# Optimization experiments

Hardware: AMD Instinct MI355X
Metric: run time of the kernel (lower is better)

## Reference

```python
import jax, jax.numpy as jnp
import numpy as np
from jax import lax

B, S, V, E, H, L = 256, 512, 32, 128, 512, 4  # batch, seq, vocab, embed, rnn_units, layers


def _lstm_bias(n4h):
    # Keras unit_forget_bias=True: forget-gate slice initialized to 1.
    b = jnp.zeros((n4h,), jnp.float32)
    return b.at[n4h // 4: n4h // 2].set(1.0)


def setup_inputs() -> dict:
    key = jax.random.key(0)
    ks = jax.random.split(key, 10)
    g = lambda k, shape, sc=0.02: (jax.random.normal(k, shape, jnp.float32) * sc)
    return dict(
        tokens=jax.random.randint(ks[0], (B, S), 0, V),
        emb=g(ks[1], (V, E), 0.05),
        w0=g(ks[2], (E, 4 * H)),
        u0=g(ks[3], (H, 4 * H)),
        b0=_lstm_bias(4 * H),
        w_rest=g(ks[4], (L - 1, H, 4 * H)),
        u_rest=g(ks[5], (L - 1, H, 4 * H)),
        b_rest=jnp.tile(_lstm_bias(4 * H)[None], (L - 1, 1)),
        dw1=g(ks[6], (H, 2 * H)),
        db1=jnp.zeros((2 * H,), jnp.float32),
        dw2=g(ks[7], (2 * H, V)),
        db2=jnp.zeros((V,), jnp.float32),
    )


def _lstm_layer(x, W, U, b):
    # x: [B,S,D]. Precompute input projection once (big GEMM), scan the recurrence.
    xz = jnp.einsum('bsd,dk->bsk', x, W) + b  # [B,S,4H]
    h0 = jnp.zeros((x.shape[0], H), x.dtype)
    c0 = jnp.zeros_like(h0)

    def step(carry, z_t):
        h, c = carry
        z = z_t + h @ U                      # [B,4H]
        i, f, g, o = jnp.split(z, 4, axis=-1)  # Keras gate order i,f,c,o
        i = jax.nn.sigmoid(i)
        f = jax.nn.sigmoid(f)
        g = jnp.tanh(g)
        o = jax.nn.sigmoid(o)
        c = f * c + i * g
        h = o * jnp.tanh(c)
        return (h, c), h

    _, hs = lax.scan(step, (h0, c0), jnp.swapaxes(xz, 0, 1))  # time-major scan
    return jnp.swapaxes(hs, 0, 1)  # [B,S,H]


def reference(tokens, emb, w0, u0, b0, w_rest, u_rest, b_rest, dw1, db1, dw2, db2):
    x = emb[tokens] * jnp.sqrt(jnp.float32(E))  # embedding scaled by sqrt(embedding_dim)
    x = _lstm_layer(x, w0, u0, b0)
    for i in range(L - 1):  # fixed small layer loop
        x = _lstm_layer(x, w_rest[i], u_rest[i], b_rest[i])
    h = jax.nn.relu(jnp.einsum('bsh,hk->bsk', x, dw1) + db1)
    return jnp.einsum('bsk,kv->bsv', h, dw2) + db2  # logits [B,S,V]
```

## Files before the change

### kernel.cpp

```cpp
#include <hip/hip_runtime.h>
#include <stdint.h>

#define NB 256
#define NS 512
#define NV 32
#define NE 128
#define NH 512
#define N4H 2048

typedef __attribute__((ext_vector_type(8))) short short8;
typedef __attribute__((ext_vector_type(4))) float f32x4;
typedef __attribute__((ext_vector_type(4))) unsigned int u32x4;
typedef __attribute__((ext_vector_type(4))) unsigned short u16x4;

__device__ __forceinline__ float bf2f(unsigned short u){
  unsigned int x = ((unsigned int)u) << 16;
  return __builtin_bit_cast(float, x);
}
__device__ __forceinline__ unsigned short f2bf(float f){
  unsigned int u = __builtin_bit_cast(unsigned int, f);
  u += 0x7fffu + ((u >> 16) & 1u);
  return (unsigned short)(u >> 16);
}
__device__ __forceinline__ void gload_lds16(const void* g, void* l){
  __builtin_amdgcn_global_load_lds(
      (const __attribute__((address_space(1))) unsigned int*)(uintptr_t)g,
      (__attribute__((address_space(3))) unsigned int*)(uintptr_t)l,
      16, 0, 0);
}

__global__ __launch_bounds__(256) void transpose_cast(
    const float* __restrict__ in, unsigned short* __restrict__ out, int K, int N)
{
  int k = blockIdx.x * 256 + threadIdx.x;
  int n = blockIdx.y;
  if (k < K) out[(long)n * K + k] = f2bf(in[(long)k * N + n]);
}

__global__ __launch_bounds__(256) void embed_kernel(
    const int* __restrict__ tok, const float* __restrict__ emb,
    unsigned short* __restrict__ x0)
{
  long gid = (long)blockIdx.x * 256 + threadIdx.x;
  long idx = gid * 4;
  int e = (int)(idx & 127);
  int b = (int)((idx >> 7) & 255);
  int t = (int)(idx >> 15);
  int tk = tok[b * NS + t];
  f32x4 v = *(const f32x4*)(emb + (long)tk * NE + e);
  u16x4 o;
  #pragma unroll
  for (int i = 0; i < 4; ++i) o[i] = f2bf(v[i] * 11.313708498984761f);
  *(u16x4*)(x0 + idx) = o;
}

template<int BM, int BN, bool BIAS, bool RELU, bool F32OUT, bool REMAP>
__global__ __launch_bounds__(256) void gemm_bt(
    const unsigned short* __restrict__ A, const unsigned short* __restrict__ BT,
    void* __restrict__ Cv, const float* __restrict__ bias,
    int M, int N, int K, int rowoff)
{
  constexpr int BK = 64;
  constexpr int WN = (BN >= 64) ? 2 : 1;
  constexpr int WM = 4 / WN;
  constexpr int WTM = BM / WM, WTN = BN / WN;
  constexpr int FM = WTM / 16, FN = WTN / 16;
  __shared__ unsigned short lds[(BM + BN) * BK];
  unsigned short* As = lds;
  unsigned short* Bs = lds + BM * BK;
  const int tid = threadIdx.x;
  const int w = tid >> 6, l = tid & 63;
  const int n0 = blockIdx.x * BN, m0 = blockIdx.y * BM;
  const int wm = (WN == 2) ? (w >> 1) : w;
  const int wn = (WN == 2) ? (w & 1) : 0;

  f32x4 acc[FM][FN];
  #pragma unroll
  for (int i = 0; i < FM; i++)
    #pragma unroll
    for (int j = 0; j < FN; j++) acc[i][j] = (f32x4)0.f;

  constexpr int CH_A = BM * 8;
  constexpr int CH_T = (BM + BN) * 8;
  constexpr int PW = CH_T / 4;
  static_assert(PW % 64 == 0, "staging alignment");
  static_assert(CH_A % 64 == 0, "region boundary alignment");

  for (int kt = 0; kt < K; kt += BK) {
    #pragma unroll
    for (int i = 0; i < PW / 64; ++i) {
      int c0 = w * PW + i * 64;
      int c = c0 + l;
      const unsigned short* g;
      if (c0 < CH_A) {
        int row = c >> 3, col = c & 7;
        g = A + (long)(m0 + row) * K + kt + col * 8;
      } else {
        int cb = c - CH_A;
        int row = cb >> 3, col = cb & 7;
        g = BT + (long)(n0 + row) * K + kt + col * 8;
      }
      gload_lds16(g, lds + (size_t)c0 * 8);
    }
    __syncthreads();
    #pragma unroll
    for (int ks = 0; ks < BK / 32; ++ks) {
      short8 a[FM], b[FN];
      #pragma unroll
      for (int mt = 0; mt < FM; ++mt)
        a[mt] = *(const short8*)&As[(wm * WTM + mt * 16 + (l & 15)) * BK + ks * 32 + (l >> 4) * 8];
      #pragma unroll
      for (int nt = 0; nt < FN; ++nt)
        b[nt] = *(const short8*)&Bs[(wn * WTN + nt * 16 + (l & 15)) * BK + ks * 32 + (l >> 4) * 8];
      #pragma unroll
      for (int mt = 0; mt < FM; ++mt)
        #pragma unroll
        for (int nt = 0; nt < FN; ++nt)
          acc[mt][nt] = __builtin_amdgcn_mfma_f32_16x16x32_bf16(a[mt], b[nt], acc[mt][nt], 0, 0, 0);
    }
    __syncthreads();
  }

  const int row_l = l >> 4, col_l = l & 15;
  #pragma unroll
  for (int nt = 0; nt < FN; ++nt) {
    int col = n0 + wn * WTN + nt * 16 + col_l;
    float bv = 0.f;
    if (BIAS) bv = bias[col];
    #pragma unroll
    for (int mt = 0; mt < FM; ++mt) {
      #pragma unroll
      for (int i = 0; i < 4; ++i) {
        int m = m0 + wm * WTM + mt * 16 + row_l * 4 + i;
        float v = acc[mt][nt][i] + bv;
        if (RELU) v = v > 0.f ? v : 0.f;
        long cidx;
        if (REMAP) {
          int gr = rowoff + m;
          int b_ = gr & (NB - 1), t_ = gr >> 8;
          cidx = ((long)b_ * NS + t_) * N + col;
        } else {
          cidx = (long)m * N + col;
        }
        if (F32OUT) ((float*)Cv)[cidx] = v;
        else ((unsigned short*)Cv)[cidx] = f2bf(v);
      }
    }
  }
}

template<int KD>
__global__ __launch_bounds__(256, 1) void lstm_scan_fused(
    const unsigned short* __restrict__ x_in,
    const unsigned short* __restrict__ WT,
    const unsigned short* __restrict__ UT,
    const float* __restrict__ bias,
    unsigned short* __restrict__ x_out,
    unsigned short* __restrict__ h_buf,
    unsigned int* __restrict__ cnt)
{
  constexpr int KS = KD / 32;
  __shared__ float Zlx[32 * 65];
  __shared__ float Zlh[32 * 65];
  __shared__ unsigned short hpack[32 * 16];

  const int tid = threadIdx.x, wv = tid >> 6, l = tid & 63;
  const int group = blockIdx.x & 7;
  const int slice = blockIdx.x >> 3;
  const int u0 = slice * 16;
  const int lr = l & 15, lk = l >> 4;
  const int j2 = tid & 15, r0 = tid >> 4;
  const int wz = wv & 1;

  short8 wfrag[2][16];
  float bv0 = 0.f, bv1 = 0.f;
  if (wv < 2) {
    #pragma unroll
    for (int g = 0; g < 2; ++g)
      #pragma unroll
      for (int ks = 0; ks < KS; ++ks)
        wfrag[g][ks] = *(const short8*)(WT + (size_t)((2 * wz + g) * NH + u0 + lr) * KD + ks * 32 + lk * 8);
    bv0 = bias[(2 * wz + 0) * NH + u0 + lr];
    bv1 = bias[(2 * wz + 1) * NH + u0 + lr];
  } else {
    #pragma unroll
    for (int g = 0; g < 2; ++g)
      #pragma unroll
      for (int ks = 0; ks < 16; ++ks)
        wfrag[g][ks] = *(const short8*)(UT + (size_t)((2 * wz + g) * NH + u0 + lr) * NH + ks * 32 + lk * 8);
  }

  short8 xa[2][16];
  const unsigned short* xp0 = x_in + (size_t)(group * 32 + lr) * KD + lk * 8;
  if (wv < 2) {
    #pragma unroll
    for (int m = 0; m < 2; ++m)
      #pragma unroll
      for (int ks = 0; ks < KS; ++ks)
        xa[m][ks] = *(const short8*)(xp0 + (size_t)m * 16 * KD + ks * 32);
  }

  unsigned short* hd0 = h_buf + group * 16384 + (slice >> 1) * 1024 + (slice & 1) * 16
                        + (l >> 1) * 32 + (l & 1) * 8;
  unsigned short* xo0 = x_out + (size_t)(group * 32 + (l >> 1)) * NH + u0 + (l & 1) * 8;
  const unsigned short* hb0 = h_buf + group * 16384 + lr * 32 + lk * 8;
  unsigned int* cp = cnt + group * 16;
  const unsigned int one = 1u;

  for (int i = tid; i < 32 * 65; i += 256) Zlh[i] = 0.f;
  __syncthreads();

  float c0 = 0.f, c1 = 0.f;

  for (int t = 0; t < NS; ++t) {
    if (wv == 0) {
      if (t > 0) {
        u32x4 hv = *(const u32x4*)((const char*)hpack + l * 16);
        unsigned short* hd = hd0 + (size_t)((t - 1) & 1) * 131072;
        asm volatile("global_store_dwordx4 %0, %1, off sc0 sc1"
                     :: "v"(hd), "v"(hv) : "memory");
        asm volatile("s_waitcnt vmcnt(0)" ::: "memory");
        if (l == 0)
          asm volatile("global_atomic_add %0, %1, off sc1"
                       :: "v"(cp), "v"(one) : "memory");
      }
    } else if (wv == 1) {
      if (t > 0) {
        u32x4 hv = *(const u32x4*)((const char*)hpack + l * 16);
        *(u32x4*)(xo0 + (size_t)(t - 1) * NB * NH) = hv;
      }
    }

    if (wv < 2) {
      f32x4 a00 = {bv0, bv0, bv0, bv0}, a01 = {bv0, bv0, bv0, bv0};
      f32x4 a10 = {bv1, bv1, bv1, bv1}, a11 = {bv1, bv1, bv1, bv1};
      #pragma unroll
      for (int ks = 0; ks < KS; ++ks) {
        a00 = __builtin_amdgcn_mfma_f32_16x16x32_bf16(xa[0][ks], wfrag[0][ks], a00, 0, 0, 0);
        a01 = __builtin_amdgcn_mfma_f32_16x16x32_bf16(xa[1][ks], wfrag[0][ks], a01, 0, 0, 0);
        a10 = __builtin_amdgcn_mfma_f32_16x16x32_bf16(xa[0][ks], wfrag[1][ks], a10, 0, 0, 0);
        a11 = __builtin_amdgcn_mfma_f32_16x16x32_bf16(xa[1][ks], wfrag[1][ks], a11, 0, 0, 0);
      }
      #pragma unroll
      for (int i = 0; i < 4; ++i) {
        Zlx[(lk * 4 + i) * 65      + (2 * wz + 0) * 16 + lr] = a00[i];
        Zlx[(16 + lk * 4 + i) * 65 + (2 * wz + 0) * 16 + lr] = a01[i];
        Zlx[(lk * 4 + i) * 65      + (2 * wz + 1) * 16 + lr] = a10[i];
        Zlx[(16 + lk * 4 + i) * 65 + (2 * wz + 1) * 16 + lr] = a11[i];
      }
      int tn = (t + 1 < NS) ? (t + 1) : t;
      const unsigned short* xp = xp0 + (size_t)tn * NB * KD;
      #pragma unroll
      for (int m = 0; m < 2; ++m)
        #pragma unroll
        for (int ks = 0; ks < KS; ++ks)
          xa[m][ks] = *(const short8*)(xp + (size_t)m * 16 * KD + ks * 32);
    } else if (t > 0) {
      {
        unsigned int v, target = 32u * (unsigned)t;
        int spin = 0;
        do {
          asm volatile("global_load_dword %0, %1, off sc0 sc1\n\ts_waitcnt vmcnt(0)"
                       : "=v"(v) : "v"(cp) : "memory");
        } while (v < target && ++spin < (1 << 15));
      }
      const unsigned short* hb_ = hb0 + (size_t)((t - 1) & 1) * 131072;
      short8 ha[2][16];
      #pragma unroll
      for (int ks = 0; ks < 16; ++ks) {
        asm volatile("global_load_dwordx4 %0, %1, off sc0 sc1"
                     : "=v"(ha[0][ks]) : "v"(hb_ + ks * 1024) : "memory");
        asm volatile("global_load_dwordx4 %0, %1, off sc0 sc1"
                     : "=v"(ha[1][ks]) : "v"(hb_ + ks * 1024 + 512) : "memory");
      }
      asm volatile("s_waitcnt vmcnt(0)" ::: "memory");
      __builtin_amdgcn_sched_barrier(0);
      f32x4 a00 = (f32x4)0.f, a01 = (f32x4)0.f, a10 = (f32x4)0.f, a11 = (f32x4)0.f;
      #pragma unroll
      for (int ks = 0; ks < 16; ++ks) {
        a00 = __builtin_amdgcn_mfma_f32_16x16x32_bf16(ha[0][ks], wfrag[0][ks], a00, 0, 0, 0);
        a01 = __builtin_amdgcn_mfma_f32_16x16x32_bf16(ha[1][ks], wfrag[0][ks], a01, 0, 0, 0);
        a10 = __builtin_amdgcn_mfma_f32_16x16x32_bf16(ha[0][ks], wfrag[1][ks], a10, 0, 0, 0);
        a11 = __builtin_amdgcn_mfma_f32_16x16x32_bf16(ha[1][ks], wfrag[1][ks], a11, 0, 0, 0);
      }
      #pragma unroll
      for (int i = 0; i < 4; ++i) {
        Zlh[(lk * 4 + i) * 65      + (2 * wz + 0) * 16 + lr] = a00[i];
        Zlh[(16 + lk * 4 + i) * 65 + (2 * wz + 0) * 16 + lr] = a01[i];
        Zlh[(lk * 4 + i) * 65      + (2 * wz + 1) * 16 + lr] = a10[i];
        Zlh[(16 + lk * 4 + i) * 65 + (2 * wz + 1) * 16 + lr] = a11[i];
      }
    }
    __syncthreads();

    #pragma unroll
    for (int p = 0; p < 2; ++p) {
      int r = r0 + p * 16;
      float zi = Zlx[r * 65 +      j2] + Zlh[r * 65 +      j2];
      float zf = Zlx[r * 65 + 16 + j2] + Zlh[r * 65 + 16 + j2];
      float zg = Zlx[r * 65 + 32 + j2] + Zlh[r * 65 + 32 + j2];
      float zo = Zlx[r * 65 + 48 + j2] + Zlh[r * 65 + 48 + j2];
      float ig = 1.f / (1.f + __expf(-zi));
      float fg = 1.f / (1.f + __expf(-zf));
      float gg = 1.f - 2.f / (__expf(2.f * zg) + 1.f);
      float og = 1.f / (1.f + __expf(-zo));
      float cc = fg * (p ? c1 : c0) + ig * gg;
      if (p) c1 = cc; else c0 = cc;
      float th = 1.f - 2.f / (__expf(2.f * cc) + 1.f);
      hpack[r * 16 + j2] = f2bf(og * th);
    }
    __syncthreads();
  }

  if (wv == 1) {
    u32x4 hv = *(const u32x4*)((const char*)hpack + l * 16);
    *(u32x4*)(xo0 + (size_t)(NS - 1) * NB * NH) = hv;
  }
}

extern "C" void kernel_launch(void* const* d_in, const int* in_sizes, int n_in,
                              void* d_out, int out_size, void* d_ws, size_t ws_size,
                              hipStream_t stream) {
  const int*   tokens = (const int*)  d_in[0];
  const float* emb    = (const float*)d_in[1];
  const float* w0     = (const float*)d_in[2];
  const float* u0     = (const float*)d_in[3];
  const float* b0     = (const float*)d_in[4];
  const float* w_rest = (const float*)d_in[5];
  const float* u_rest = (const float*)d_in[6];
  const float* b_rest = (const float*)d_in[7];
  const float* dw1    = (const float*)d_in[8];
  const float* db1    = (const float*)d_in[9];
  const float* dw2    = (const float*)d_in[10];
  const float* db2    = (const float*)d_in[11];
  float* out = (float*)d_out;

  char* ws = (char*)d_ws;
  size_t off = 0;
  auto alloc = [&](size_t bytes) -> char* {
    char* p = ws + off;
    off += (bytes + 255) & ~(size_t)255;
    return p;
  };
  unsigned short* ut[4];
  for (int i = 0; i < 4; ++i) ut[i] = (unsigned short*)alloc((size_t)N4H * NH * 2);
  unsigned short* w0t = (unsigned short*)alloc((size_t)N4H * NE * 2);
  unsigned short* wt[3];
  for (int i = 0; i < 3; ++i) wt[i] = (unsigned short*)alloc((size_t)N4H * NH * 2);
  unsigned short* dw1t = (unsigned short*)alloc((size_t)1024 * 512 * 2);
  unsigned short* dw2t = (unsigned short*)alloc((size_t)32 * 1024 * 2);
  unsigned short* x0  = (unsigned short*)alloc((size_t)NB * NS * NE * 2);
  unsigned short* xA  = (unsigned short*)alloc((size_t)NB * NS * NH * 2);
  unsigned short* hb  = (unsigned short*)alloc((size_t)2 * 8 * 16384 * 2);
  unsigned int*  cnt  = (unsigned int*)alloc((size_t)4 * 8 * 16 * 4);

  size_t avail = (ws_size > off) ? (ws_size - off) : 0;
  long RC = (long)(avail / ((size_t)1024 * 2));
  if (RC > (long)NB * NS) RC = (long)NB * NS;
  RC &= ~(long)127;
  if (RC < 128) RC = 128;
  unsigned short* h1buf = (unsigned short*)alloc((size_t)RC * 1024 * 2);

  (void)hipMemsetAsync(cnt, 0, (size_t)4 * 8 * 16 * 4, stream);

  transpose_cast<<<dim3(1, N4H), 256, 0, stream>>>(w0, w0t, NE, N4H);
  transpose_cast<<<dim3(2, N4H), 256, 0, stream>>>(u0, ut[0], NH, N4H);
  for (int i = 0; i < 3; ++i) {
    transpose_cast<<<dim3(2, N4H), 256, 0, stream>>>(w_rest + (size_t)i * NH * N4H, wt[i], NH, N4H);
    transpose_cast<<<dim3(2, N4H), 256, 0, stream>>>(u_rest + (size_t)i * NH * N4H, ut[i + 1], NH, N4H);
  }
  transpose_cast<<<dim3(2, 1024), 256, 0, stream>>>(dw1, dw1t, 512, 1024);
  transpose_cast<<<dim3(4, 32), 256, 0, stream>>>(dw2, dw2t, 1024, 32);

  embed_kernel<<<16384, 256, 0, stream>>>(tokens, emb, x0);

  lstm_scan_fused<NE><<<256, 256, 0, stream>>>(
      x0, w0t, ut[0], b0, xA, hb, cnt);
  for (int lyr = 1; lyr < 4; ++lyr) {
    lstm_scan_fused<NH><<<256, 256, 0, stream>>>(
        xA, wt[lyr - 1], ut[lyr], b_rest + (size_t)(lyr - 1) * N4H, xA, hb,
        cnt + (size_t)lyr * 8 * 16);
  }

  for (long r0 = 0; r0 < (long)NB * NS; r0 += RC) {
    long rows = ((long)NB * NS - r0 < RC) ? ((long)NB * NS - r0) : RC;
    gemm_bt<128, 128, true, true, false, false>
        <<<dim3(1024 / 128, rows / 128), 256, 0, stream>>>(
            xA + (size_t)r0 * NH, dw1t, h1buf, db1, (int)rows, 1024, NH, 0);
    gemm_bt<128, 32, true, false, true, true>
        <<<dim3(1, rows / 128), 256, 0, stream>>>(
            h1buf, dw2t, out, db2, (int)rows, 32, 1024, (int)r0);
  }
}
```

Before: 13.95 ms.

## Replace atomic counter barrier with per-block sequence flags and direct h publish

Each block now writes its new h values straight to the global exchange buffer and to the layer output right after the gate math, then publishes a per-block sequence number. This replaces the delayed hpack-staged store plus an atomic add on a shared counter. Consumers poll the 32 per-slice flags of their group with a wave-wide check. The kernel also requests 96KB of dynamic LDS, apparently to force one block per CU. The aim is to take a full step of latency and atomic contention out of the recurrent critical path, at the cost of many scattered 2-byte stores.

```diff
diff --git a/kernel.cpp b/kernel.cpp
--- a/kernel.cpp
+++ b/kernel.cpp
@@ -149,6 +149,8 @@
   }
 }
 
+#define SCAN_LDS_BYTES 98304
+
 template<int KD>
 __global__ __launch_bounds__(256, 1) void lstm_scan_fused(
     const unsigned short* __restrict__ x_in,
@@ -157,12 +159,12 @@
     const float* __restrict__ bias,
     unsigned short* __restrict__ x_out,
     unsigned short* __restrict__ h_buf,
-    unsigned int* __restrict__ cnt)
+    unsigned int* __restrict__ seq)
 {
   constexpr int KS = KD / 32;
-  __shared__ float Zlx[32 * 65];
-  __shared__ float Zlh[32 * 65];
-  __shared__ unsigned short hpack[32 * 16];
+  extern __shared__ char smem[];
+  float* Zlx = (float*)smem;
+  float* Zlh = (float*)(smem + 8448);
 
   const int tid = threadIdx.x, wv = tid >> 6, l = tid & 63;
   const int group = blockIdx.x & 7;
@@ -170,6 +172,7 @@
   const int u0 = slice * 16;
   const int lr = l & 15, lk = l >> 4;
   const int j2 = tid & 15, r0 = tid >> 4;
+  const int n_ = u0 + j2;
   const int wz = wv & 1;
 
   short8 wfrag[2][16];
@@ -190,7 +193,7 @@
         wfrag[g][ks] = *(const short8*)(UT + (size_t)((2 * wz + g) * NH + u0 + lr) * NH + ks * 32 + lk * 8);
   }
 
-  short8 xa[2][16];
+  short8 xa[2][KS];
   const unsigned short* xp0 = x_in + (size_t)(group * 32 + lr) * KD + lk * 8;
   if (wv < 2) {
     #pragma unroll
@@ -200,12 +203,11 @@
         xa[m][ks] = *(const short8*)(xp0 + (size_t)m * 16 * KD + ks * 32);
   }
 
-  unsigned short* hd0 = h_buf + group * 16384 + (slice >> 1) * 1024 + (slice & 1) * 16
-                        + (l >> 1) * 32 + (l & 1) * 8;
-  unsigned short* xo0 = x_out + (size_t)(group * 32 + (l >> 1)) * NH + u0 + (l & 1) * 8;
+  const int hpub = group * 16384 + (slice >> 1) * 1024 + r0 * 32 + (slice & 1) * 16 + j2;
   const unsigned short* hb0 = h_buf + group * 16384 + lr * 32 + lk * 8;
-  unsigned int* cp = cnt + group * 16;
-  const unsigned int one = 1u;
+  unsigned int* seqline = seq + group * 32;
+  unsigned int* myseq = seqline + slice;
+  const unsigned int* fp = seqline + (l & 31);
 
   for (int i = tid; i < 32 * 65; i += 256) Zlh[i] = 0.f;
   __syncthreads();
@@ -213,24 +215,6 @@
   float c0 = 0.f, c1 = 0.f;
 
   for (int t = 0; t < NS; ++t) {
-    if (wv == 0) {
-      if (t > 0) {
-        u32x4 hv = *(const u32x4*)((const char*)hpack + l * 16);
-        unsigned short* hd = hd0 + (size_t)((t - 1) & 1) * 131072;
-        asm volatile("global_store_dwordx4 %0, %1, off sc0 sc1"
-                     :: "v"(hd), "v"(hv) : "memory");
-        asm volatile("s_waitcnt vmcnt(0)" ::: "memory");
-        if (l == 0)
-          asm volatile("global_atomic_add %0, %1, off sc1"
-                       :: "v"(cp), "v"(one) : "memory");
-      }
-    } else if (wv == 1) {
-      if (t > 0) {
-        u32x4 hv = *(const u32x4*)((const char*)hpack + l * 16);
-        *(u32x4*)(xo0 + (size_t)(t - 1) * NB * NH) = hv;
-      }
-    }
-
     if (wv < 2) {
       f32x4 a00 = {bv0, bv0, bv0, bv0}, a01 = {bv0, bv0, bv0, bv0};
       f32x4 a10 = {bv1, bv1, bv1, bv1}, a11 = {bv1, bv1, bv1, bv1};
@@ -257,12 +241,11 @@
           xa[m][ks] = *(const short8*)(xp + (size_t)m * 16 * KD + ks * 32);
     } else if (t > 0) {
       {
-        unsigned int v, target = 32u * (unsigned)t;
-        int spin = 0;
+        unsigned int v; int spin = 0;
         do {
           asm volatile("global_load_dword %0, %1, off sc0 sc1\n\ts_waitcnt vmcnt(0)"
-                       : "=v"(v) : "v"(cp) : "memory");
-        } while (v < target && ++spin < (1 << 15));
+                       : "=v"(v) : "v"(fp) : "memory");
+        } while (!__all(v >= (unsigned)t) && ++spin < (1 << 15));
       }
       const unsigned short* hb_ = hb0 + (size_t)((t - 1) & 1) * 131072;
       short8 ha[2][16];
@@ -293,6 +276,7 @@
     }
     __syncthreads();
 
+    unsigned short hsh[2];
     #pragma unroll
     for (int p = 0; p < 2; ++p) {
       int r = r0 + p * 16;
@@ -307,14 +291,25 @@
       float cc = fg * (p ? c1 : c0) + ig * gg;
       if (p) c1 = cc; else c0 = cc;
       float th = 1.f - 2.f / (__expf(2.f * cc) + 1.f);
-      hpack[r * 16 + j2] = f2bf(og * th);
+      hsh[p] = f2bf(og * th);
+    }
+    {
+      unsigned short* hp = h_buf + (size_t)(t & 1) * 131072 + hpub;
+      unsigned int s0 = hsh[0], s1 = hsh[1];
+      asm volatile("global_store_short %0, %1, off sc0 sc1"
+                   :: "v"(hp), "v"(s0) : "memory");
+      asm volatile("global_store_short %0, %1, off sc0 sc1"
+                   :: "v"(hp + 512), "v"(s1) : "memory");
+      x_out[((size_t)t * NB + group * 32 + r0) * NH + n_] = hsh[0];
+      x_out[((size_t)t * NB + group * 32 + r0 + 16) * NH + n_] = hsh[1];
+      asm volatile("s_waitcnt vmcnt(0)" ::: "memory");
     }
     __syncthreads();
-  }
-
-  if (wv == 1) {
-    u32x4 hv = *(const u32x4*)((const char*)hpack + l * 16);
-    *(u32x4*)(xo0 + (size_t)(NS - 1) * NB * NH) = hv;
+    if (tid == 0) {
+      unsigned int nv = (unsigned int)(t + 1);
+      asm volatile("global_store_dword %0, %1, off sc0 sc1"
+                   :: "v"(myseq), "v"(nv) : "memory");
+    }
   }
 }
 
@@ -352,7 +347,7 @@
   unsigned short* x0  = (unsigned short*)alloc((size_t)NB * NS * NE * 2);
   unsigned short* xA  = (unsigned short*)alloc((size_t)NB * NS * NH * 2);
   unsigned short* hb  = (unsigned short*)alloc((size_t)2 * 8 * 16384 * 2);
-  unsigned int*  cnt  = (unsigned int*)alloc((size_t)4 * 8 * 16 * 4);
+  unsigned int*  seq  = (unsigned int*)alloc((size_t)4 * 8 * 32 * 4);
 
   size_t avail = (ws_size > off) ? (ws_size - off) : 0;
   long RC = (long)(avail / ((size_t)1024 * 2));
@@ -361,7 +356,7 @@
   if (RC < 128) RC = 128;
   unsigned short* h1buf = (unsigned short*)alloc((size_t)RC * 1024 * 2);
 
-  (void)hipMemsetAsync(cnt, 0, (size_t)4 * 8 * 16 * 4, stream);
+  (void)hipMemsetAsync(seq, 0, (size_t)4 * 8 * 32 * 4, stream);
 
   transpose_cast<<<dim3(1, N4H), 256, 0, stream>>>(w0, w0t, NE, N4H);
   transpose_cast<<<dim3(2, N4H), 256, 0, stream>>>(u0, ut[0], NH, N4H);
@@ -374,12 +369,17 @@
 
   embed_kernel<<<16384, 256, 0, stream>>>(tokens, emb, x0);
 
-  lstm_scan_fused<NE><<<256, 256, 0, stream>>>(
-      x0, w0t, ut[0], b0, xA, hb, cnt);
+  (void)hipFuncSetAttribute((const void*)lstm_scan_fused<NE>,
+                            hipFuncAttributeMaxDynamicSharedMemorySize, SCAN_LDS_BYTES);
+  (void)hipFuncSetAttribute((const void*)lstm_scan_fused<NH>,
+                            hipFuncAttributeMaxDynamicSharedMemorySize, SCAN_LDS_BYTES);
+
+  lstm_scan_fused<NE><<<256, 256, SCAN_LDS_BYTES, stream>>>(
+      x0, w0t, ut[0], b0, xA, hb, seq);
   for (int lyr = 1; lyr < 4; ++lyr) {
-    lstm_scan_fused<NH><<<256, 256, 0, stream>>>(
+    lstm_scan_fused<NH><<<256, 256, SCAN_LDS_BYTES, stream>>>(
         xA, wt[lyr - 1], ut[lyr], b_rest + (size_t)(lyr - 1) * N4H, xA, hb,
-        cnt + (size_t)lyr * 8 * 16);
+        seq + (size_t)lyr * 8 * 32);
   }
 
   for (long r0 = 0; r0 < (long)NB * NS; r0 += RC) {
```

Measured after the change: 11.50 ms. 17.5% less time.
